# Kernel tuning notes

Hardware: AMD Instinct MI355X
Metric: run time of the kernel (lower is better)

## Reference

```python
import jax, jax.numpy as jnp
import numpy as np
from jax import lax

INF = 1e6  # stand-in for infinity; INF**2 = 1e12 fits comfortably in fp32


def _boundary_3x3(targets):
    """morphological_gradient(size=(3,3)) > 0 on int label maps [B,H,W].
    scipy default mode='reflect' with pad width 1 == edge padding."""
    B, H, W = targets.shape
    p = jnp.pad(targets, ((0, 0), (1, 1), (1, 1)), mode='edge')
    patches = jnp.stack([p[:, i:i + H, j:j + W]
                         for i in range(3) for j in range(3)], axis=0)
    return (patches.max(0) - patches.min(0)) > 0  # [B,H,W] bool


def _row_dist(boundary):
    """Per-row 1D distance (in column index) to nearest boundary pixel. [B,H,W] float."""
    B, H, W = boundary.shape
    bT = jnp.moveaxis(boundary, 2, 0)  # [W,B,H]

    def step(c, b):
        c = jnp.where(b, 0.0, jnp.minimum(c + 1.0, INF))
        return c, c

    init = jnp.full((B, H), INF, dtype=jnp.float32)
    _, fwd = lax.scan(step, init, bT)
    _, bwd = lax.scan(step, init, bT[::-1])
    g = jnp.minimum(fwd, bwd[::-1])  # [W,B,H]
    return jnp.moveaxis(g, 0, 2)  # [B,H,W]


def _edt(boundary):
    """Exact 2D Euclidean distance transform to the boundary set (separable form):
    d(i,j)^2 = min_k ( (i-k)^2 + g(k,j)^2 )."""
    B, H, W = boundary.shape
    g2 = _row_dist(boundary) ** 2  # [B,H,W]
    ii = jnp.arange(H, dtype=jnp.float32)
    dk2 = (ii[:, None] - ii[None, :]) ** 2  # [H_i, H_k]
    # [B, H_i, H_k, W] -> min over k
    d2 = jnp.min(dk2[None, :, :, None] + g2[:, None, :, :], axis=2)
    return jnp.sqrt(d2)


def boundary_weight(targets, sigma):
    boundary = _boundary_3x3(targets)
    dist = _edt(boundary)
    w = jnp.exp(-dist / sigma)
    has_b = boundary.any(axis=(1, 2))[:, None, None]
    return jnp.where(has_b, w, 1.0)  # all-ones map if no boundary


def setup_inputs() -> dict:
    key = jax.random.key(0)
    k1, k2 = jax.random.split(key)
    B, C, H, W = 8, 19, 256, 256
    inputs = jax.random.normal(k1, (B, C, H, W), dtype=jnp.float32)
    targets = jax.random.randint(k2, (B, H, W), 0, C, dtype=jnp.int32)
    return {"inputs": inputs, "targets": targets}


def reference(inputs, targets):
    sigma = 5.0
    logp = jax.nn.log_softmax(inputs, axis=1)  # [B,C,H,W]
    ce = -jnp.take_along_axis(logp, targets[:, None, :, :], axis=1)[:, 0]  # [B,H,W]
    w = boundary_weight(targets, sigma)
    return (ce * w).mean()
```

## Files before the change

kernel.cpp:

```cpp
#include <hip/hip_runtime.h>

#define BB 8
#define CC 19
#define HH 256
#define WW 256
#define HWW 65536
#define IT 8
#define BIGF 3.0e12f


__global__ __launch_bounds__(256) void k_bnd_ce(
    const float* __restrict__ x, const int* __restrict__ tgt,
    float* __restrict__ g2, float* __restrict__ ce,
    int* __restrict__ rowany, float* __restrict__ out)
{
    const int blk = blockIdx.x;
    const int b   = blk >> 6;
    const int i0  = (blk & 63) << 2;
    const int j   = threadIdx.x;

    __shared__ int trow[6][WW];
    __shared__ int bflag[4][WW];
    __shared__ int s_any;

    if (blk == 0 && j == 0) out[0] = 0.0f;
    if (j == 0) s_any = 0;

    const int* tbase = tgt + b * HWW;
#pragma unroll
    for (int rr = 0; rr < 6; ++rr) {
        int hh = min(max(i0 - 1 + rr, 0), HH - 1);
        trow[rr][j] = tbase[hh * WW + j];
    }
    __syncthreads();

    const int r  = j >> 6;
    const int c0 = (j & 63) << 2;
    const int h  = i0 + r;

    int anyb = 0;
#pragma unroll
    for (int t = 0; t < 4; ++t) {
        int c = c0 + t;
        int cm = max(c - 1, 0), cp = min(c + 1, WW - 1);
        int mx = trow[r][cm], mn = mx;
#pragma unroll
        for (int rr = 0; rr < 3; ++rr) {
            int a0 = trow[r + rr][cm], a1 = trow[r + rr][c], a2 = trow[r + rr][cp];
            mx = max(mx, max(a0, max(a1, a2)));
            mn = min(mn, min(a0, min(a1, a2)));
        }
        int bnd = (mx != mn) ? 1 : 0;
        bflag[r][c] = bnd;
        anyb |= bnd;
    }
    unsigned long long msk = __ballot(anyb);
    if ((j & 63) == 0 && msk) s_any = 1;
    __syncthreads();
    if (j == 0) rowany[blk] = s_any;

    float4 g4;
    float* gp = (float*)&g4;
#pragma unroll
    for (int t = 0; t < 4; ++t) {
        int c = c0 + t;
        float mind = 1e6f;
        for (int d = 0; d < WW; ++d) {
            int lo = c - d, hi = c + d;
            if ((lo >= 0 && bflag[r][lo]) || (hi < WW && bflag[r][hi])) {
                mind = (float)d; break;
            }
        }
        gp[t] = mind * mind;
    }
    *(float4*)(g2 + (size_t)(b * HH + h) * WW + c0) = g4;

    const float* px = x + ((size_t)(b * CC) * HH + h) * WW + c0;
    float4 s4 = make_float4(0.f, 0.f, 0.f, 0.f);
#pragma unroll
    for (int c = 0; c < CC; ++c) {
        float4 v = *(const float4*)(px + (size_t)c * HWW);
        s4.x += expf(v.x); s4.y += expf(v.y);
        s4.z += expf(v.z); s4.w += expf(v.w);
    }
    const int t0 = trow[r + 1][c0],     t1 = trow[r + 1][c0 + 1],
              t2 = trow[r + 1][c0 + 2], t3 = trow[r + 1][c0 + 3];
    float4 c4;
    c4.x = logf(s4.x) - px[(size_t)t0 * HWW + 0];
    c4.y = logf(s4.y) - px[(size_t)t1 * HWW + 1];
    c4.z = logf(s4.z) - px[(size_t)t2 * HWW + 2];
    c4.w = logf(s4.w) - px[(size_t)t3 * HWW + 3];
    *(float4*)(ce + (size_t)(b * HH + h) * WW + c0) = c4;
}

__global__ __launch_bounds__(256) void k_edt_red(
    const float* __restrict__ g2, const float* __restrict__ ce,
    const int* __restrict__ rowany, float* __restrict__ out)
{
    const int b  = blockIdx.x >> 5;
    const int i0 = (blockIdx.x & 31) * IT;
    const int j  = threadIdx.x;

    __shared__ int s_has;
    __shared__ float wsum[4];
    if (j == 0) s_has = 0;
    int ra = (j < 64) ? rowany[b * 64 + j] : 0;
    unsigned long long mk = __ballot(ra != 0);
    __syncthreads();
    if ((j & 63) == 0 && mk) s_has = 1;
    __syncthreads();
    const int has = s_has;

    float md[IT];
#pragma unroll
    for (int r = 0; r < IT; ++r) md[r] = BIGF;
    const float* gcol = g2 + (size_t)b * HWW + j;
    const int c0 = i0 + 4;
    for (int d0 = 0; d0 < HH; d0 += 4) {
        float gl[4], gr[4];
        int   kl[4], kr[4];
#pragma unroll
        for (int t = 0; t < 4; ++t) {
            int d = d0 + t;
            kl[t] = c0 - d; kr[t] = c0 + d;
            gl[t] = (kl[t] >= 0 && kl[t] < HH) ? gcol[(size_t)kl[t] * WW] : BIGF;
            gr[t] = (kr[t] >= 0 && kr[t] < HH) ? gcol[(size_t)kr[t] * WW] : BIGF;
        }
#pragma unroll
        for (int t = 0; t < 4; ++t) {
#pragma unroll
            for (int r = 0; r < IT; ++r) {
                float dl = (float)(i0 + r - kl[t]);
                float dr = (float)(i0 + r - kr[t]);
                md[r] = fminf(md[r], fmaf(dl, dl, gl[t]));
                md[r] = fminf(md[r], fmaf(dr, dr, gr[t]));
            }
        }
        float bm = md[0];
#pragma unroll
        for (int r = 1; r < IT; ++r) bm = fmaxf(bm, md[r]);
        float fut = (float)(d0 * d0);
        if (fut > bm) break;
    }

    float acc = 0.0f;
#pragma unroll
    for (int r = 0; r < IT; ++r) {
        float dist = sqrtf(md[r]);
        float w = has ? expf(-dist / 5.0f) : 1.0f;
        acc += ce[((size_t)b * HH + i0 + r) * WW + j] * w;
    }

    for (int off = 32; off > 0; off >>= 1)
        acc += __shfl_down(acc, off, 64);
    const int lane = j & 63, wid = j >> 6;
    if (lane == 0) wsum[wid] = acc;
    __syncthreads();
    if (j == 0) {
        float tot = wsum[0] + wsum[1] + wsum[2] + wsum[3];
        atomicAdd(out, tot * (1.0f / (float)(BB * HWW)));
    }
}

extern "C" void kernel_launch(void* const* d_in, const int* in_sizes, int n_in,
                              void* d_out, int out_size, void* d_ws, size_t ws_size,
                              hipStream_t stream) {
    const float* x   = (const float*)d_in[0];
    const int*   tgt = (const int*)d_in[1];
    float*       out = (float*)d_out;

    char* ws = (char*)d_ws;
    float* g2     = (float*)ws;
    float* ce     = (float*)(ws + (size_t)BB * HWW * sizeof(float));
    int*   rowany = (int*)  (ws + (size_t)2 * BB * HWW * sizeof(float));

    k_bnd_ce <<<BB * (HH / 4), 256, 0, stream>>>(x, tgt, g2, ce, rowany, out);
    k_edt_red<<<BB * (HH / IT), 256, 0, stream>>>(g2, ce, rowany, out);
}
```

Baseline: 86.99 us.

## Move cross-entropy into EDT kernel and drop ce/rowany intermediate buffers

Splits the work differently. The first kernel now computes only boundary flags and row distances. The second kernel loads the 19 logits per pixel, computes cross-entropy in registers, and runs the column EDT with float4 loads over 4 columns per thread. This removes the ce write/read round trip and the rowany ballot. It replaces the has-boundary flag with a sentinel test on the distance, and selects the target logit in registers instead of doing a gather. Holding 19 float4 values in registers raises register pressure. The EDT early exit is now per thread rather than per 8-row tile, which may add divergence and more g2 loads.

New measurement: 89.26 us. 2.6% more time.

```diff
diff --git a/kernel.cpp b/kernel.cpp
--- a/kernel.cpp
+++ b/kernel.cpp
@@ -5,14 +5,12 @@
 #define HH 256
 #define WW 256
 #define HWW 65536
-#define IT 8
 #define BIGF 3.0e12f
+#define SENT 1.0e11f
 
 
-__global__ __launch_bounds__(256) void k_bnd_ce(
-    const float* __restrict__ x, const int* __restrict__ tgt,
-    float* __restrict__ g2, float* __restrict__ ce,
-    int* __restrict__ rowany, float* __restrict__ out)
+__global__ __launch_bounds__(256) void k_g2(
+    const int* __restrict__ tgt, float* __restrict__ g2, float* __restrict__ out)
 {
     const int blk = blockIdx.x;
     const int b   = blk >> 6;
@@ -21,10 +19,8 @@
 
     __shared__ int trow[6][WW];
     __shared__ int bflag[4][WW];
-    __shared__ int s_any;
 
     if (blk == 0 && j == 0) out[0] = 0.0f;
-    if (j == 0) s_any = 0;
 
     const int* tbase = tgt + b * HWW;
 #pragma unroll
@@ -38,7 +34,6 @@
     const int c0 = (j & 63) << 2;
     const int h  = i0 + r;
 
-    int anyb = 0;
 #pragma unroll
     for (int t = 0; t < 4; ++t) {
         int c = c0 + t;
@@ -50,14 +45,9 @@
             mx = max(mx, max(a0, max(a1, a2)));
             mn = min(mn, min(a0, min(a1, a2)));
         }
-        int bnd = (mx != mn) ? 1 : 0;
-        bflag[r][c] = bnd;
-        anyb |= bnd;
+        bflag[r][c] = (mx != mn) ? 1 : 0;
     }
-    unsigned long long msk = __ballot(anyb);
-    if ((j & 63) == 0 && msk) s_any = 1;
     __syncthreads();
-    if (j == 0) rowany[blk] = s_any;
 
     float4 g4;
     float* gp = (float*)&g4;
@@ -74,82 +64,78 @@
         gp[t] = mind * mind;
     }
     *(float4*)(g2 + (size_t)(b * HH + h) * WW + c0) = g4;
+}
+
+__global__ __launch_bounds__(256) void k_ce_edt(
+    const float* __restrict__ x, const int* __restrict__ tgt,
+    const float* __restrict__ g2, float* __restrict__ out)
+{
+    const int blk = blockIdx.x;
+    const int b   = blk >> 6;
+    const int i0  = (blk & 63) << 2;
+    const int j   = threadIdx.x;
+
+    __shared__ float wsum[4];
+
+    const int r  = j >> 6;
+    const int c0 = (j & 63) << 2;
+    const int h  = i0 + r;
 
     const float* px = x + ((size_t)(b * CC) * HH + h) * WW + c0;
-    float4 s4 = make_float4(0.f, 0.f, 0.f, 0.f);
+    float4 v[CC];
 #pragma unroll
-    for (int c = 0; c < CC; ++c) {
-        float4 v = *(const float4*)(px + (size_t)c * HWW);
-        s4.x += expf(v.x); s4.y += expf(v.y);
-        s4.z += expf(v.z); s4.w += expf(v.w);
-    }
-    const int t0 = trow[r + 1][c0],     t1 = trow[r + 1][c0 + 1],
-              t2 = trow[r + 1][c0 + 2], t3 = trow[r + 1][c0 + 3];
-    float4 c4;
-    c4.x = logf(s4.x) - px[(size_t)t0 * HWW + 0];
-    c4.y = logf(s4.y) - px[(size_t)t1 * HWW + 1];
-    c4.z = logf(s4.z) - px[(size_t)t2 * HWW + 2];
-    c4.w = logf(s4.w) - px[(size_t)t3 * HWW + 3];
-    *(float4*)(ce + (size_t)(b * HH + h) * WW + c0) = c4;
-}
+    for (int c = 0; c < CC; ++c)
+        v[c] = *(const float4*)(px + (size_t)c * HWW);
 
-__global__ __launch_bounds__(256) void k_edt_red(
-    const float* __restrict__ g2, const float* __restrict__ ce,
-    const int* __restrict__ rowany, float* __restrict__ out)
-{
-    const int b  = blockIdx.x >> 5;
-    const int i0 = (blockIdx.x & 31) * IT;
-    const int j  = threadIdx.x;
+    const int4 t4 = *(const int4*)(tgt + b * HWW + h * WW + c0);
 
-    __shared__ int s_has;
-    __shared__ float wsum[4];
-    if (j == 0) s_has = 0;
-    int ra = (j < 64) ? rowany[b * 64 + j] : 0;
-    unsigned long long mk = __ballot(ra != 0);
-    __syncthreads();
-    if ((j & 63) == 0 && mk) s_has = 1;
-    __syncthreads();
-    const int has = s_has;
-
-    float md[IT];
-#pragma unroll
-    for (int r = 0; r < IT; ++r) md[r] = BIGF;
-    const float* gcol = g2 + (size_t)b * HWW + j;
-    const int c0 = i0 + 4;
+    const float* gimg = g2 + (size_t)b * HWW;
+    float md0 = BIGF, md1 = BIGF, md2 = BIGF, md3 = BIGF;
     for (int d0 = 0; d0 < HH; d0 += 4) {
-        float gl[4], gr[4];
-        int   kl[4], kr[4];
 #pragma unroll
         for (int t = 0; t < 4; ++t) {
             int d = d0 + t;
-            kl[t] = c0 - d; kr[t] = c0 + d;
-            gl[t] = (kl[t] >= 0 && kl[t] < HH) ? gcol[(size_t)kl[t] * WW] : BIGF;
-            gr[t] = (kr[t] >= 0 && kr[t] < HH) ? gcol[(size_t)kr[t] * WW] : BIGF;
-        }
-#pragma unroll
-        for (int t = 0; t < 4; ++t) {
-#pragma unroll
-            for (int r = 0; r < IT; ++r) {
-                float dl = (float)(i0 + r - kl[t]);
-                float dr = (float)(i0 + r - kr[t]);
-                md[r] = fminf(md[r], fmaf(dl, dl, gl[t]));
-                md[r] = fminf(md[r], fmaf(dr, dr, gr[t]));
+            float fd2 = (float)(d * d);
+            int ku = h - d, kd = h + d;
+            if (ku >= 0) {
+                float4 gu = *(const float4*)(gimg + (size_t)ku * WW + c0);
+                md0 = fminf(md0, gu.x + fd2);
+                md1 = fminf(md1, gu.y + fd2);
+                md2 = fminf(md2, gu.z + fd2);
+                md3 = fminf(md3, gu.w + fd2);
+            }
+            if (d > 0 && kd < HH) {
+                float4 gd = *(const float4*)(gimg + (size_t)kd * WW + c0);
+                md0 = fminf(md0, gd.x + fd2);
+                md1 = fminf(md1, gd.y + fd2);
+                md2 = fminf(md2, gd.z + fd2);
+                md3 = fminf(md3, gd.w + fd2);
             }
         }
-        float bm = md[0];
-#pragma unroll
-        for (int r = 1; r < IT; ++r) bm = fmaxf(bm, md[r]);
-        float fut = (float)(d0 * d0);
+        float bm = fmaxf(fmaxf(md0, md1), fmaxf(md2, md3));
+        float fut = (float)((d0 + 4) * (d0 + 4));
         if (fut > bm) break;
     }
 
-    float acc = 0.0f;
+    float4 s4 = make_float4(0.f, 0.f, 0.f, 0.f);
+    float xv0 = 0.f, xv1 = 0.f, xv2 = 0.f, xv3 = 0.f;
 #pragma unroll
-    for (int r = 0; r < IT; ++r) {
-        float dist = sqrtf(md[r]);
-        float w = has ? expf(-dist / 5.0f) : 1.0f;
-        acc += ce[((size_t)b * HH + i0 + r) * WW + j] * w;
+    for (int c = 0; c < CC; ++c) {
+        s4.x += expf(v[c].x); s4.y += expf(v[c].y);
+        s4.z += expf(v[c].z); s4.w += expf(v[c].w);
+        xv0 = (c == t4.x) ? v[c].x : xv0;
+        xv1 = (c == t4.y) ? v[c].y : xv1;
+        xv2 = (c == t4.z) ? v[c].z : xv2;
+        xv3 = (c == t4.w) ? v[c].w : xv3;
     }
+    const float ce0 = logf(s4.x) - xv0, ce1 = logf(s4.y) - xv1,
+                ce2 = logf(s4.z) - xv2, ce3 = logf(s4.w) - xv3;
+
+    const float w0 = (md0 < SENT) ? expf(-sqrtf(md0) / 5.0f) : 1.0f;
+    const float w1 = (md1 < SENT) ? expf(-sqrtf(md1) / 5.0f) : 1.0f;
+    const float w2 = (md2 < SENT) ? expf(-sqrtf(md2) / 5.0f) : 1.0f;
+    const float w3 = (md3 < SENT) ? expf(-sqrtf(md3) / 5.0f) : 1.0f;
+    float acc = ce0 * w0; acc += ce1 * w1; acc += ce2 * w2; acc += ce3 * w3;
 
     for (int off = 32; off > 0; off >>= 1)
         acc += __shfl_down(acc, off, 64);
@@ -169,11 +155,8 @@
     const int*   tgt = (const int*)d_in[1];
     float*       out = (float*)d_out;
 
-    char* ws = (char*)d_ws;
-    float* g2     = (float*)ws;
-    float* ce     = (float*)(ws + (size_t)BB * HWW * sizeof(float));
-    int*   rowany = (int*)  (ws + (size_t)2 * BB * HWW * sizeof(float));
+    float* g2 = (float*)d_ws;
 
-    k_bnd_ce <<<BB * (HH / 4), 256, 0, stream>>>(x, tgt, g2, ce, rowany, out);
-    k_edt_red<<<BB * (HH / IT), 256, 0, stream>>>(g2, ce, rowany, out);
+    k_g2    <<<BB * (HH / 4), 256, 0, stream>>>(tgt, g2, out);
+    k_ce_edt<<<BB * (HH / 4), 256, 0, stream>>>(x, tgt, g2, out);
 }
```
